# Kernel optimization log

Measured on AMD Instinct MI355X. Metric: run time of the kernel, lower is better.

The kernel has to match this reference:

```python
import jax, jax.numpy as jnp
import numpy as np

H_D, W_D = 64, 64          # 1024x1024 image / 16 patch size
N = H_D * W_D              # 4096 patches
D = 768                    # DINO ViT-B/16 embed dim
ALPHA = 0.5
K = 100


def setup_inputs() -> dict:
    key = jax.random.key(0)
    k1, k2 = jax.random.split(key)
    out = jax.random.normal(k1, (N, D), dtype=jnp.float32)
    attn_seed = jax.random.randint(k2, (2,), 0, H_D, dtype=jnp.int32)
    return {"out": out, "attn_seed": attn_seed}


def _connected_components(mask):
    """8-connectivity connected components via iterative min-label propagation.
    Background = 0. Foreground pixels get the minimum initial id (+1) of their
    component (same partition as cv2.connectedComponents, different numbering)."""
    fg = mask > 0
    BIG = jnp.int32(N + 1)
    init = jnp.where(fg, jnp.arange(N, dtype=jnp.int32).reshape(H_D, W_D) + 1, BIG)

    def step(l):
        p = jnp.pad(l, 1, constant_values=N + 1)
        m = l
        for dy in (0, 1, 2):          # fixed 3x3 neighborhood, not a data-dim loop
            for dx in (0, 1, 2):
                m = jnp.minimum(m, p[dy:dy + H_D, dx:dx + W_D])
        return jnp.where(fg, m, BIG)

    def cond(st):
        l, prev = st
        return jnp.any(l != prev)

    def body(st):
        l, _ = st
        return step(l), l

    l, _ = jax.lax.while_loop(cond, body, (step(init), init))
    return jnp.where(fg, l, 0)


def reference(out, attn_seed):
    # similarity between all patch features: [N, N]
    sim = out @ out.T
    deg = sim >= 0                                        # degree_matrix (bool)
    # patch with fewest non-negative similarities
    seed_degree_flat = jnp.argmin(deg.sum(axis=0)).astype(jnp.int32)
    seed_degree = jnp.stack([seed_degree_flat // W_D, seed_degree_flat % W_D])
    # blend degree seed with attention seed
    seed_rc = jnp.round(ALPHA * seed_degree + (1.0 - ALPHA) * attn_seed).astype(jnp.int32)
    seed = seed_rc[0] * W_D + seed_rc[1]

    # initial expansion set = patches positively correlated with the seed
    s = deg[seed].astype(jnp.int32)
    s = s.at[seed].set(1)                                 # degree_matrix[seed][seed] = 255 (truthy)
    order = jnp.argsort(-sim[seed])                       # descending
    s = s.at[order[K:]].set(0)                            # keep top-k most similar

    # sequential seed expansion (updates feed into later iterations)
    def step(s, i):
        grows = jnp.sum(sim[i] * (s == 1)) > 0
        s = s.at[i].set(jnp.where(s[i] == 0, 0, jnp.where(grows, 1, 0)))
        return s, None

    s, _ = jax.lax.scan(step, s, jnp.arange(N))

    return _connected_components(s.reshape(H_D, W_D))
```

## Files before the change

### kernel.cpp

```cpp
#include <hip/hip_runtime.h>
#include <cstdint>

#define NP   4096
#define DD   768
#define HD   64
#define WD   64
#define KTOP 100
#define BIGL 4097

typedef short bf16x8 __attribute__((ext_vector_type(8)));
typedef float f32x4  __attribute__((ext_vector_type(4)));

__device__ __forceinline__ void gload_lds16(const void* g, void* l) {
    __builtin_amdgcn_global_load_lds(
        (const __attribute__((address_space(1))) unsigned int*)(uintptr_t)g,
        (__attribute__((address_space(3))) unsigned int*)(unsigned int)(uintptr_t)l,
        16, 0, 0);
}

__device__ __forceinline__ unsigned short f2bf_rne(float x) {
    unsigned b = __float_as_uint(x);
    unsigned r = b + 0x7FFFu + ((b >> 16) & 1u);
    return (unsigned short)(r >> 16);
}
__device__ __forceinline__ float bf2f(unsigned short h) {
    return __uint_as_float(((unsigned)h) << 16);
}

__global__ __launch_bounds__(256) void k_split(const float* __restrict__ A,
                                               unsigned short* __restrict__ hi,
                                               unsigned short* __restrict__ lo,
                                               int* __restrict__ counts) {
    if (blockIdx.x < 16) counts[blockIdx.x * 256 + threadIdx.x] = 0;
    int idx = blockIdx.x * 256 + threadIdx.x;
    float4 v = ((const float4*)A)[idx];
    unsigned short h0 = f2bf_rne(v.x), h1 = f2bf_rne(v.y),
                   h2 = f2bf_rne(v.z), h3 = f2bf_rne(v.w);
    unsigned short l0 = f2bf_rne(v.x - bf2f(h0)), l1 = f2bf_rne(v.y - bf2f(h1)),
                   l2 = f2bf_rne(v.z - bf2f(h2)), l3 = f2bf_rne(v.w - bf2f(h3));
    ((ushort4*)hi)[idx] = make_ushort4(h0, h1, h2, h3);
    ((ushort4*)lo)[idx] = make_ushort4(l0, l1, l2, l3);
}

__device__ __forceinline__ void stage_group(const unsigned short* __restrict__ hi,
                                            const unsigned short* __restrict__ lo,
                                            int i0, int j0, int kbase, int tid,
                                            unsigned short* G) {
#pragma unroll
    for (int q = 0; q < 4; ++q) {
        int pp = q * 512 + tid;
        int ppt = pp & 1023;
        int row = ppt >> 3;
        int kcl = (ppt & 7) ^ (row & 7);
        int rbase = (pp < 1024) ? i0 : j0;
        const unsigned short* src =
            ((kcl < 4) ? hi : lo) + (size_t)(rbase + row) * DD + kbase + (kcl & 3) * 8;
        gload_lds16(src, G + pp * 8);
    }
}

__global__ __launch_bounds__(512, 4) void k_gemm(const unsigned short* __restrict__ hi,
                                                 const unsigned short* __restrict__ lo,
                                                 int* __restrict__ counts) {
    __shared__ __align__(16) unsigned short G[2][2048 * 8];
    __shared__ int colc[128];
    __shared__ int rowc[128];

    int t = ((blockIdx.x & 7) * 66) + (blockIdx.x >> 3);
    int SI = 0, SJ = 0, rem = t;
    for (;;) {
        int sz = (SI == SJ) ? 36 : 64;
        if (rem < sz) break;
        rem -= sz;
        if (++SJ == 4) { ++SI; SJ = SI; }
    }
    int li, lj;
    if (SI == SJ) {
        int r = 0;
        while (rem >= (8 - r)) { rem -= (8 - r); ++r; }
        li = r; lj = r + rem;
    } else { li = rem >> 3; lj = rem & 7; }
    int bi = SI * 8 + li, bj = SJ * 8 + lj;
    int i0 = bi * 128, j0 = bj * 128;

    int tid = threadIdx.x;
    int lane = tid & 63, w = tid >> 6;
    int wm = w & 1, wn = w >> 1;

    f32x4 acc[4][2];
#pragma unroll
    for (int ti = 0; ti < 4; ++ti)
#pragma unroll
        for (int u = 0; u < 2; ++u) { acc[ti][u][0] = 0.f; acc[ti][u][1] = 0.f;
                                      acc[ti][u][2] = 0.f; acc[ti][u][3] = 0.f; }

    int kcf = lane >> 4;
    int paH[4], paL[4], pbH[2], pbL[2];
#pragma unroll
    for (int tt = 0; tt < 4; ++tt) {
        int arow = wm * 64 + tt * 16 + (lane & 15);
        paH[tt] = arow * 8 + (kcf ^ (arow & 7));
        paL[tt] = arow * 8 + ((kcf + 4) ^ (arow & 7));
    }
#pragma unroll
    for (int u = 0; u < 2; ++u) {
        int brow = wn * 32 + u * 16 + (lane & 15);
        pbH[u] = 1024 + brow * 8 + (kcf ^ (brow & 7));
        pbL[u] = 1024 + brow * 8 + ((kcf + 4) ^ (brow & 7));
    }

    stage_group(hi, lo, i0, j0, 0, tid, G[0]);
    for (int it = 0; it < 24; ++it) {
        int cur = it & 1;
        __syncthreads();
        if (it + 1 < 24)
            stage_group(hi, lo, i0, j0, (it + 1) * 32, tid, G[cur ^ 1]);
        bf16x8 ahi[4], alo[4], bhi[2], blo[2];
#pragma unroll
        for (int tt = 0; tt < 4; ++tt) {
            ahi[tt] = *(const bf16x8*)&G[cur][paH[tt] * 8];
            alo[tt] = *(const bf16x8*)&G[cur][paL[tt] * 8];
        }
#pragma unroll
        for (int u = 0; u < 2; ++u) {
            bhi[u] = *(const bf16x8*)&G[cur][pbH[u] * 8];
            blo[u] = *(const bf16x8*)&G[cur][pbL[u] * 8];
        }
#pragma unroll
        for (int ti = 0; ti < 4; ++ti)
#pragma unroll
            for (int u = 0; u < 2; ++u) {
                acc[ti][u] = __builtin_amdgcn_mfma_f32_16x16x32_bf16(
                    ahi[ti], bhi[u], acc[ti][u], 0, 0, 0);
                acc[ti][u] = __builtin_amdgcn_mfma_f32_16x16x32_bf16(
                    alo[ti], bhi[u], acc[ti][u], 0, 0, 0);
                acc[ti][u] = __builtin_amdgcn_mfma_f32_16x16x32_bf16(
                    ahi[ti], blo[u], acc[ti][u], 0, 0, 0);
            }
    }

    if (tid < 128) { colc[tid] = 0; rowc[tid] = 0; }
    __syncthreads();

    int nl = lane & 15;
    int rg = lane >> 4;
    int cc[2] = {0, 0};
#pragma unroll
    for (int ti = 0; ti < 4; ++ti)
#pragma unroll
        for (int u = 0; u < 2; ++u) {
            f32x4 a = acc[ti][u];
            cc[u] += ((a[0] >= 0.f) ? 1 : 0) + ((a[1] >= 0.f) ? 1 : 0) +
                     ((a[2] >= 0.f) ? 1 : 0) + ((a[3] >= 0.f) ? 1 : 0);
        }
#pragma unroll
    for (int u = 0; u < 2; ++u) {
        int v = cc[u];
        v += __shfl_xor(v, 16);
        v += __shfl_xor(v, 32);
        if (rg == 0) atomicAdd(&colc[wn * 32 + u * 16 + nl], v);
    }
    if (bi != bj) {
#pragma unroll
        for (int ti = 0; ti < 4; ++ti)
#pragma unroll
            for (int g = 0; g < 4; ++g) {
                int rv = ((acc[ti][0][g] >= 0.f) ? 1 : 0) +
                         ((acc[ti][1][g] >= 0.f) ? 1 : 0);
                rv += __shfl_xor(rv, 1);
                rv += __shfl_xor(rv, 2);
                rv += __shfl_xor(rv, 4);
                rv += __shfl_xor(rv, 8);
                if (nl == 0) atomicAdd(&rowc[wm * 64 + ti * 16 + rg * 4 + g], rv);
            }
    }
    __syncthreads();
    if (tid < 128) {
        atomicAdd(&counts[j0 + tid], colc[tid]);
        if (bi != bj) atomicAdd(&counts[i0 + tid], rowc[tid]);
    }
}

__device__ __forceinline__ int block_sum256(int v, int lane, int w, int* wred) {
#pragma unroll
    for (int o = 1; o < 64; o <<= 1) v += __shfl_xor(v, o);
    if (lane == 0) wred[w] = v;
    __syncthreads();
    int tt = wred[0] + wred[1] + wred[2] + wred[3];
    __syncthreads();
    return tt;
}
__device__ __forceinline__ int block_exscan256(int v, int lane, int w, int* wred,
                                               int* total) {
    int inc = v;
#pragma unroll
    for (int o = 1; o < 64; o <<= 1) { int u = __shfl_up(inc, o); if (lane >= o) inc += u; }
    if (lane == 63) wred[w] = inc;
    __syncthreads();
    int w0 = wred[0], w1 = wred[1], w2 = wred[2], w3 = wred[3];
    int wofs = (w > 0 ? w0 : 0) + (w > 1 ? w1 : 0) + (w > 2 ? w2 : 0);
    *total = w0 + w1 + w2 + w3;
    __syncthreads();
    return wofs + inc - v;
}

__global__ __launch_bounds__(256) void k_seedrow(const float* __restrict__ A,
                                                 const int* __restrict__ counts,
                                                 const int* __restrict__ attn_seed,
                                                 float* __restrict__ simrow,
                                                 int* __restrict__ seedp,
                                                 int* __restrict__ outp) {
    __shared__ int redA[256], redB[256];
    int tid = threadIdx.x, lane = tid & 63, w = tid >> 6;
    int blk = blockIdx.x;

    int bc = 0x7fffffff, bI = 0;
    for (int j = tid; j < NP; j += 256) {
        int c = counts[j];
        if (c < bc) { bc = c; bI = j; }
    }
    redA[tid] = bc; redB[tid] = bI;
    __syncthreads();
    for (int st = 128; st > 0; st >>= 1) {
        if (tid < st) {
            if (redA[tid + st] < redA[tid] ||
                (redA[tid + st] == redA[tid] && redB[tid + st] < redB[tid])) {
                redA[tid] = redA[tid + st];
                redB[tid] = redB[tid + st];
            }
        }
        __syncthreads();
    }
    int flat = redB[0];
    int sr = flat / WD, sc = flat % WD;
    int vr = sr + attn_seed[0];
    int vc = sc + attn_seed[1];
    int rr, rc;
    if ((vr & 1) == 0) rr = vr >> 1;
    else { int m = vr >> 1; rr = (m & 1) ? m + 1 : m; }
    if ((vc & 1) == 0) rc = vc >> 1;
    else { int m = vc >> 1; rc = (m & 1) ? m + 1 : m; }
    int seed = rr * WD + rc;
    if (blk == 0 && tid == 0) seedp[0] = seed;

    float sv[12];
#pragma unroll
    for (int kk = 0; kk < 12; ++kk) sv[kk] = A[(size_t)seed * DD + lane + kk * 64];
    int jbase = blk * 32 + w * 8;
    for (int jj = 0; jj < 8; ++jj) {
        int j = jbase + jj;
        float sum = 0.f;
#pragma unroll
        for (int kk = 0; kk < 12; ++kk)
            sum += sv[kk] * A[(size_t)j * DD + lane + kk * 64];
#pragma unroll
        for (int o = 32; o > 0; o >>= 1) sum += __shfl_down(sum, o);
        if (lane == 0) simrow[j] = sum;
    }
    if (tid < 32) outp[blk * 32 + tid] = 0;
}

__global__ __launch_bounds__(256) void k_sel(const float* __restrict__ simrow,
                                             const int* __restrict__ seedp,
                                             int* __restrict__ act, int* __restrict__ Mp) {
    __shared__ int wred[4];
    int tid = threadIdx.x, lane = tid & 63, w = tid >> 6;
    int seed = seedp[0];
    int base = tid * 16;
    unsigned key[16];
#pragma unroll
    for (int n = 0; n < 16; ++n) {
        unsigned b = __float_as_uint(simrow[base + n]);
        key[n] = (b & 0x80000000u) ? ~b : (b | 0x80000000u);
    }
    unsigned prefix = 0;
    for (int bit = 31; bit >= 0; --bit) {
        unsigned cand = prefix | (1u << bit);
        int c = 0;
#pragma unroll
        for (int n = 0; n < 16; ++n) c += (key[n] >= cand) ? 1 : 0;
        int tot = block_sum256(c, lane, w, wred);
        if (tot >= KTOP) prefix = cand;
    }
    unsigned KT = prefix;
    int cgt = 0, ceq = 0;
#pragma unroll
    for (int n = 0; n < 16; ++n) {
        cgt += (key[n] > KT) ? 1 : 0;
        ceq += (key[n] == KT) ? 1 : 0;
    }
    int totgt = block_sum256(cgt, lane, w, wred);
    int slots = KTOP - totgt;
    int dummy;
    int eqrun = block_exscan256(ceq, lane, w, wred, &dummy);
    int flag[16]; int cf = 0;
#pragma unroll
    for (int n = 0; n < 16; ++n) {
        int j = base + n;
        unsigned k = key[n];
        int topk = (k > KT) || (k == KT && eqrun < slots);
        if (k == KT) ++eqrun;
        int f = (topk && (k >= 0x80000000u || j == seed)) ? 1 : 0;
        flag[n] = f; cf += f;
    }
    int M;
    int off = block_exscan256(cf, lane, w, wred, &M);
    if (tid == 0) Mp[0] = M;
#pragma unroll
    for (int n = 0; n < 16; ++n)
        if (flag[n]) act[off++] = base + n;
}

__global__ __launch_bounds__(256) void k_sub(const float* __restrict__ A,
                                             const int* __restrict__ act,
                                             const int* __restrict__ Mp,
                                             float* __restrict__ subsim) {
    __shared__ float av[DD];
    int M = Mp[0];
    int p = blockIdx.x;
    if (p >= M) return;
    int tid = threadIdx.x, lane = tid & 63, w = tid >> 6;
    int ip = act[p];
    for (int k = tid; k < DD; k += 256) av[k] = A[(size_t)ip * DD + k];
    __syncthreads();
    for (int q = w; q < M; q += 4) {
        int iq = act[q];
        float sum = 0.f;
#pragma unroll
        for (int kk = 0; kk < 12; ++kk) {
            int k = lane + kk * 64;
            sum += av[k] * A[(size_t)iq * DD + k];
        }
#pragma unroll
        for (int o = 32; o > 0; o >>= 1) sum += __shfl_down(sum, o);
        if (lane == 0) subsim[p * 128 + q] = sum;
    }
}

__global__ __launch_bounds__(256) void k_fin(const float* __restrict__ subsim,
                                             const int* __restrict__ act,
                                             const int* __restrict__ Mp,
                                             int* __restrict__ outp) {
    __shared__ float ss[128 * 128];
    __shared__ int act_s[128];
    __shared__ int alive[128];
    __shared__ int lab[128];
    __shared__ unsigned char nbr[128][8];
    __shared__ int ncnt[128];
    __shared__ int chg;
    int M = Mp[0];
    int tid = threadIdx.x, lane = tid & 63;

    if (tid < 128) act_s[tid] = (tid < M) ? act[tid] : 0;
    for (int idx = tid; idx < M * 128; idx += 256) {
        int p = idx >> 7, q = idx & 127;
        ss[q * 128 + ((p + q) & 127)] = subsim[idx];
    }
    __syncthreads();

    if (tid < 64) {
        float S_lo = 0.f, S_hi = 0.f;
        for (int q = 0; q < M; ++q) {
            S_lo += ss[q * 128 + ((lane + q) & 127)];
            S_hi += ss[q * 128 + ((lane + 64 + q) & 127)];
        }
        float al = (lane < M) ? 1.f : 0.f;
        float ah = (lane + 64 < M) ? 1.f : 0.f;
        for (int p = 0; p < M; ++p) {
            float Sp = (p < 64) ? __shfl(S_lo, p) : __shfl(S_hi, p - 64);
            if (!(Sp > 0.f)) {
                S_lo -= ss[p * 128 + ((lane + p) & 127)];
                S_hi -= ss[p * 128 + ((lane + 64 + p) & 127)];
                if (lane == p)      al = 0.f;
                if (lane + 64 == p) ah = 0.f;
            }
        }
        alive[lane]      = (lane < M && al != 0.f) ? 1 : 0;
        alive[lane + 64] = (lane + 64 < M && ah != 0.f) ? 1 : 0;
    }
    __syncthreads();

    if (tid < 128) {
        int a = (tid < M) ? alive[tid] : 0;
        int c = 0;
        if (a) {
            int id = act_s[tid];
            int y = id >> 6, x = id & 63;
            for (int q = 0; q < M; ++q) {
                if (q == tid || !alive[q]) continue;
                int qid = act_s[q];
                int dy = (qid >> 6) - y, dx = (qid & 63) - x;
                if (dy >= -1 && dy <= 1 && dx >= -1 && dx <= 1)
                    nbr[tid][c++] = (unsigned char)q;
            }
        }
        ncnt[tid] = c;
        lab[tid] = a ? tid : 32767;
    }
    __syncthreads();
    while (true) {
        if (tid == 0) chg = 0;
        __syncthreads();
        int local = 0;
        if (tid < M && alive[tid]) {
            int m = lab[tid];
            int nc = ncnt[tid];
            for (int k = 0; k < nc; ++k) { int u = lab[nbr[tid][k]]; if (u < m) m = u; }
            { int u = lab[m]; if (u < m) m = u; }
            { int u = lab[m]; if (u < m) m = u; }
            if (m < lab[tid]) { lab[tid] = m; local = 1; }
        }
        if (local) chg = 1;
        __syncthreads();
        if (chg == 0) break;
        __syncthreads();
    }
    if (tid < M && alive[tid]) outp[act_s[tid]] = act_s[lab[tid]] + 1;
}

extern "C" void kernel_launch(void* const* d_in, const int* in_sizes, int n_in,
                              void* d_out, int out_size, void* d_ws, size_t ws_size,
                              hipStream_t stream) {
    const float* A = (const float*)d_in[0];
    const int* attn = (const int*)d_in[1];
    int* outp = (int*)d_out;

    char* ws = (char*)d_ws;
    int*            counts = (int*)(ws);
    float*          simrow = (float*)(ws + 16384);
    int*            act    = (int*)(ws + 32768);
    int*            Mp     = (int*)(ws + 33280);
    int*            seedp  = (int*)(ws + 33284);
    float*          subsim = (float*)(ws + 33792);
    unsigned short* hi     = (unsigned short*)(ws + 1048576);
    unsigned short* lo     = (unsigned short*)(ws + 1048576 + 6291456);

    k_split  <<<3072, 256, 0, stream>>>(A, hi, lo, counts);
    k_gemm   <<<528,  512, 0, stream>>>(hi, lo, counts);
    k_seedrow<<<128,  256, 0, stream>>>(A, counts, attn, simrow, seedp, outp);
    k_sel    <<<1,    256, 0, stream>>>(simrow, seedp, act, Mp);
    k_sub    <<<128,  256, 0, stream>>>(A, act, Mp, subsim);
    k_fin    <<<1,    256, 0, stream>>>(subsim, act, Mp, outp);
}
```

Before: 190.8 us.

## Use 4 waves with 64x64 per-wave tiles and explicit waitcnt pipelining in GEMM

The symmetric-tile GEMM now runs 256 threads per block instead of 512, so each wave computes a 64x64 sub-tile (4x4 MFMA tiles) and reuses its A and B fragments across more MFMAs. The single __syncthreads is replaced by explicit vmcnt/lgkmcnt waits with raw barriers, so the next stage's global-to-LDS loads stay in flight during compute, and s_setprio raises wave priority around the MFMA block. The final kernel also reads subsim with float4 loads. In exchange, each wave holds twice as many accumulator registers and fewer waves are available to hide latency.

```diff
diff --git a/kernel.cpp b/kernel.cpp
--- a/kernel.cpp
+++ b/kernel.cpp
@@ -47,8 +47,8 @@
                                             int i0, int j0, int kbase, int tid,
                                             unsigned short* G) {
 #pragma unroll
-    for (int q = 0; q < 4; ++q) {
-        int pp = q * 512 + tid;
+    for (int q = 0; q < 8; ++q) {
+        int pp = q * 256 + tid;
         int ppt = pp & 1023;
         int row = ppt >> 3;
         int kcl = (ppt & 7) ^ (row & 7);
@@ -59,7 +59,7 @@
     }
 }
 
-__global__ __launch_bounds__(512, 4) void k_gemm(const unsigned short* __restrict__ hi,
+__global__ __launch_bounds__(256, 2) void k_gemm(const unsigned short* __restrict__ hi,
                                                  const unsigned short* __restrict__ lo,
                                                  int* __restrict__ counts) {
     __shared__ __align__(16) unsigned short G[2][2048 * 8];
@@ -87,15 +87,15 @@
     int lane = tid & 63, w = tid >> 6;
     int wm = w & 1, wn = w >> 1;
 
-    f32x4 acc[4][2];
+    f32x4 acc[4][4];
 #pragma unroll
     for (int ti = 0; ti < 4; ++ti)
 #pragma unroll
-        for (int u = 0; u < 2; ++u) { acc[ti][u][0] = 0.f; acc[ti][u][1] = 0.f;
+        for (int u = 0; u < 4; ++u) { acc[ti][u][0] = 0.f; acc[ti][u][1] = 0.f;
                                       acc[ti][u][2] = 0.f; acc[ti][u][3] = 0.f; }
 
     int kcf = lane >> 4;
-    int paH[4], paL[4], pbH[2], pbL[2];
+    int paH[4], paL[4], pbH[4], pbL[4];
 #pragma unroll
     for (int tt = 0; tt < 4; ++tt) {
         int arow = wm * 64 + tt * 16 + (lane & 15);
@@ -103,8 +103,8 @@
         paL[tt] = arow * 8 + ((kcf + 4) ^ (arow & 7));
     }
 #pragma unroll
-    for (int u = 0; u < 2; ++u) {
-        int brow = wn * 32 + u * 16 + (lane & 15);
+    for (int u = 0; u < 4; ++u) {
+        int brow = wn * 64 + u * 16 + (lane & 15);
         pbH[u] = 1024 + brow * 8 + (kcf ^ (brow & 7));
         pbL[u] = 1024 + brow * 8 + ((kcf + 4) ^ (brow & 7));
     }
@@ -112,24 +112,33 @@
     stage_group(hi, lo, i0, j0, 0, tid, G[0]);
     for (int it = 0; it < 24; ++it) {
         int cur = it & 1;
-        __syncthreads();
-        if (it + 1 < 24)
+        if (it < 23) {
             stage_group(hi, lo, i0, j0, (it + 1) * 32, tid, G[cur ^ 1]);
-        bf16x8 ahi[4], alo[4], bhi[2], blo[2];
+            asm volatile("s_waitcnt vmcnt(8)" ::: "memory");
+        } else {
+            asm volatile("s_waitcnt vmcnt(0)" ::: "memory");
+        }
+        __builtin_amdgcn_s_barrier();
+
+        bf16x8 ahi[4], alo[4], bhi[4], blo[4];
 #pragma unroll
         for (int tt = 0; tt < 4; ++tt) {
             ahi[tt] = *(const bf16x8*)&G[cur][paH[tt] * 8];
             alo[tt] = *(const bf16x8*)&G[cur][paL[tt] * 8];
         }
 #pragma unroll
-        for (int u = 0; u < 2; ++u) {
+        for (int u = 0; u < 4; ++u) {
             bhi[u] = *(const bf16x8*)&G[cur][pbH[u] * 8];
             blo[u] = *(const bf16x8*)&G[cur][pbL[u] * 8];
         }
+        asm volatile("s_waitcnt lgkmcnt(0)" ::: "memory");
+        __builtin_amdgcn_s_barrier();
+
+        __builtin_amdgcn_s_setprio(1);
 #pragma unroll
         for (int ti = 0; ti < 4; ++ti)
 #pragma unroll
-            for (int u = 0; u < 2; ++u) {
+            for (int u = 0; u < 4; ++u) {
                 acc[ti][u] = __builtin_amdgcn_mfma_f32_16x16x32_bf16(
                     ahi[ti], bhi[u], acc[ti][u], 0, 0, 0);
                 acc[ti][u] = __builtin_amdgcn_mfma_f32_16x16x32_bf16(
@@ -137,6 +146,7 @@
                 acc[ti][u] = __builtin_amdgcn_mfma_f32_16x16x32_bf16(
                     ahi[ti], blo[u], acc[ti][u], 0, 0, 0);
             }
+        __builtin_amdgcn_s_setprio(0);
     }
 
     if (tid < 128) { colc[tid] = 0; rowc[tid] = 0; }
@@ -144,21 +154,18 @@
 
     int nl = lane & 15;
     int rg = lane >> 4;
-    int cc[2] = {0, 0};
-#pragma unroll
-    for (int ti = 0; ti < 4; ++ti)
-#pragma unroll
-        for (int u = 0; u < 2; ++u) {
+#pragma unroll
+    for (int u = 0; u < 4; ++u) {
+        int v = 0;
+#pragma unroll
+        for (int ti = 0; ti < 4; ++ti) {
             f32x4 a = acc[ti][u];
-            cc[u] += ((a[0] >= 0.f) ? 1 : 0) + ((a[1] >= 0.f) ? 1 : 0) +
-                     ((a[2] >= 0.f) ? 1 : 0) + ((a[3] >= 0.f) ? 1 : 0);
-        }
-#pragma unroll
-    for (int u = 0; u < 2; ++u) {
-        int v = cc[u];
+            v += ((a[0] >= 0.f) ? 1 : 0) + ((a[1] >= 0.f) ? 1 : 0) +
+                 ((a[2] >= 0.f) ? 1 : 0) + ((a[3] >= 0.f) ? 1 : 0);
+        }
         v += __shfl_xor(v, 16);
         v += __shfl_xor(v, 32);
-        if (rg == 0) atomicAdd(&colc[wn * 32 + u * 16 + nl], v);
+        if (rg == 0) atomicAdd(&colc[wn * 64 + u * 16 + nl], v);
     }
     if (bi != bj) {
 #pragma unroll
@@ -166,7 +173,9 @@
 #pragma unroll
             for (int g = 0; g < 4; ++g) {
                 int rv = ((acc[ti][0][g] >= 0.f) ? 1 : 0) +
-                         ((acc[ti][1][g] >= 0.f) ? 1 : 0);
+                         ((acc[ti][1][g] >= 0.f) ? 1 : 0) +
+                         ((acc[ti][2][g] >= 0.f) ? 1 : 0) +
+                         ((acc[ti][3][g] >= 0.f) ? 1 : 0);
                 rv += __shfl_xor(rv, 1);
                 rv += __shfl_xor(rv, 2);
                 rv += __shfl_xor(rv, 4);
@@ -351,10 +360,14 @@
     int M = Mp[0];
     int tid = threadIdx.x, lane = tid & 63;
 
-    if (tid < 128) act_s[tid] = (tid < M) ? act[tid] : 0;
-    for (int idx = tid; idx < M * 128; idx += 256) {
-        int p = idx >> 7, q = idx & 127;
-        ss[q * 128 + ((p + q) & 127)] = subsim[idx];
+    if (tid < 128) act_s[tid] = (tid < 128 && tid < M) ? act[tid] : 0;
+    for (int i4 = tid; i4 < M * 32; i4 += 256) {
+        int p = i4 >> 5, qb = (i4 & 31) << 2;
+        float4 v = ((const float4*)subsim)[i4];
+        ss[(qb + 0) * 128 + ((p + qb + 0) & 127)] = v.x;
+        ss[(qb + 1) * 128 + ((p + qb + 1) & 127)] = v.y;
+        ss[(qb + 2) * 128 + ((p + qb + 2) & 127)] = v.z;
+        ss[(qb + 3) * 128 + ((p + qb + 3) & 127)] = v.w;
     }
     __syncthreads();
 
@@ -436,7 +449,7 @@
     unsigned short* lo     = (unsigned short*)(ws + 1048576 + 6291456);
 
     k_split  <<<3072, 256, 0, stream>>>(A, hi, lo, counts);
-    k_gemm   <<<528,  512, 0, stream>>>(hi, lo, counts);
+    k_gemm   <<<528,  256, 0, stream>>>(hi, lo, counts);
     k_seedrow<<<128,  256, 0, stream>>>(A, counts, attn, simrow, seedp, outp);
     k_sel    <<<1,    256, 0, stream>>>(simrow, seedp, act, Mp);
     k_sub    <<<128,  256, 0, stream>>>(A, act, Mp, subsim);
```

Result: no change. 193.8 us (+1.6%).
